# Performance work log

Hardware: AMD Instinct MI355X
Metric: run time of the kernel (lower is better)

Reference implementation:

```python
import jax, jax.numpy as jnp
import numpy as np

NUM_HEADS = 12
N_SAMPLE = 60
COS_LOW = 0.7
COS_HIGH = 0.9
EPS = 1e-12  # F.normalize eps


def _l2norm(x, axis=-1):
    n = jnp.linalg.norm(x, axis=axis, keepdims=True)
    return x / jnp.maximum(n, EPS)


def get_random_attn(rng, v, n_sample, cos_low, cos_high):
    # v: (B, S) -- the CLS attention-score row per batch-head
    norm = jnp.linalg.norm(v, axis=-1, keepdims=True)            # (B, 1)
    u = _l2norm(v)                                               # (B, S)
    u = jnp.broadcast_to(u[None], (n_sample,) + v.shape)         # (n, B, S)
    k1, k2 = jax.random.split(rng)
    r = jax.random.uniform(k1, u.shape, dtype=v.dtype) * 2 - 1   # (n, B, S)
    a = jnp.einsum('nbd,nbd->nb', r, u)[..., None]               # (n, B, 1)
    uperp = _l2norm(r - a * u)                                   # (n, B, S)
    cos = (jax.random.uniform(k2, (n_sample,), dtype=v.dtype)
           * (cos_high - cos_low) + cos_low)[:, None, None]      # (n, 1, 1)
    w = cos * u + jnp.sqrt(1 - cos ** 2) * uperp                 # (n, B, S)
    return jnp.transpose(w * norm[None], (1, 0, 2))              # (B, n, S)


def setup_inputs() -> dict:
    key = jax.random.key(0)
    ks = jax.random.split(key, 8)
    L, N, E = 197, 128, 768
    s = 0.02
    return {
        'query': jax.random.normal(ks[0], (L, N, E), jnp.float32),
        'key': jax.random.normal(ks[1], (L, N, E), jnp.float32),
        'value': jax.random.normal(ks[2], (L, N, E), jnp.float32),
        'in_proj_weight': jax.random.normal(ks[3], (3 * E, E), jnp.float32) * s,
        'in_proj_bias': jax.random.normal(ks[4], (3 * E,), jnp.float32) * s,
        'out_proj_weight': jax.random.normal(ks[5], (E, E), jnp.float32) * s,
        'out_proj_bias': jax.random.normal(ks[6], (E,), jnp.float32) * s,
    }


def reference(query, key, value, in_proj_weight, in_proj_bias,
              out_proj_weight, out_proj_bias):
    L, N, E = query.shape
    H = NUM_HEADS
    hd = E // H
    # packed in-projection (separate q/k/v tensors -> chunked weights)
    w_q, w_k, w_v = jnp.split(in_proj_weight, 3, axis=0)
    b_q, b_k, b_v = jnp.split(in_proj_bias, 3, axis=0)
    q = query @ w_q.T + b_q
    k = key @ w_k.T + b_k
    v = value @ w_v.T + b_v
    # (L, N, E) -> (N*H, L, hd)
    q = jnp.transpose(q.reshape(L, N * H, hd), (1, 0, 2))
    k = jnp.transpose(k.reshape(L, N * H, hd), (1, 0, 2))
    v = jnp.transpose(v.reshape(L, N * H, hd), (1, 0, 2))
    q = q / jnp.sqrt(jnp.asarray(hd, q.dtype))
    attn = jnp.einsum('bte,bse->bts', q, k)                      # (B, L, S)
    center = attn[:, 0, :]                                        # (B, S)
    rand_rows = get_random_attn(jax.random.key(1234), center,
                                N_SAMPLE, COS_LOW, COS_HIGH)      # (B, n, S)
    attn = jnp.concatenate([attn[:, :1, :], rand_rows, attn[:, 1:, :]], axis=1)
    attn = jax.nn.softmax(attn, axis=-1)                          # (B, L+n, S)
    out = jnp.einsum('bts,bse->bte', attn, v)                     # (B, L+n, hd)
    Lt = L + N_SAMPLE
    out = jnp.transpose(out, (1, 0, 2)).reshape(Lt, N, E)
    out = out @ out_proj_weight.T + out_proj_bias                 # (Lt, N, E)
    attn_weights = attn.reshape(N, H, Lt, L).mean(axis=1)         # averaged heads
    return out, attn_weights
```

## Files before the change

### kernel.cpp

```cpp
#include <hip/hip_runtime.h>
#include <stdint.h>

constexpr int Lc  = 197;
constexpr int Nc  = 128;
constexpr int Ec  = 768;
constexpr int HDc = 64;
constexpr int Bc  = Nc * 12;
constexpr int LTc = Lc + 60;
constexpr float EPSc = 1e-12f;

struct U2 { uint32_t x, y; };

__device__ __forceinline__ U2 tf2x32(uint32_t k0, uint32_t k1, uint32_t x0, uint32_t x1) {
  uint32_t k2 = k0 ^ k1 ^ 0x1BD11BDAu;
  x0 += k0; x1 += k1;
#define TFR(r) { x0 += x1; x1 = (x1 << (r)) | (x1 >> (32 - (r))); x1 ^= x0; }
  TFR(13) TFR(15) TFR(26) TFR(6)
  x0 += k1; x1 += k2 + 1u;
  TFR(17) TFR(29) TFR(16) TFR(24)
  x0 += k2; x1 += k0 + 2u;
  TFR(13) TFR(15) TFR(26) TFR(6)
  x0 += k0; x1 += k1 + 3u;
  TFR(17) TFR(29) TFR(16) TFR(24)
  x0 += k1; x1 += k2 + 4u;
  TFR(13) TFR(15) TFR(26) TFR(6)
  x0 += k2; x1 += k0 + 5u;
#undef TFR
  return {x0, x1};
}

__device__ __forceinline__ float u01f(uint32_t bits) {
  return __uint_as_float((bits >> 9) | 0x3f800000u) - 1.0f;
}

__device__ __forceinline__ uint32_t rbits(uint32_t ka, uint32_t kb, uint32_t idx) {
  U2 r = tf2x32(ka, kb, 0u, idx);
  return r.x ^ r.y;
}

__device__ __forceinline__ void split_keys(uint32_t& k1a, uint32_t& k1b, uint32_t& k2a, uint32_t& k2b) {
  U2 t0 = tf2x32(0u, 1234u, 0u, 0u); k1a = t0.x; k1b = t0.y;
  U2 t1 = tf2x32(0u, 1234u, 0u, 1u); k2a = t1.x; k2b = t1.y;
}

__device__ __forceinline__ float rdlane(float v, int l) {
  return __int_as_float(__builtin_amdgcn_readlane(__float_as_int(v), l));
}

__device__ __forceinline__ void f2hilo(float f, unsigned short& h, unsigned short& l) {
  uint32_t u = __float_as_uint(f);
  h = (unsigned short)(u >> 16);
  float lof = f - __uint_as_float(u & 0xffff0000u);
  l = (unsigned short)(__float_as_uint(lof) >> 16);
}

__global__ __launch_bounds__(256) void convert_hilo(const float* __restrict__ src,
                                                    unsigned short* __restrict__ dst,
                                                    int rows)
{
  int idx = blockIdx.x * 256 + threadIdx.x;
  int total = rows * 192;
  if (idx >= total) return;
  int m = idx / 192, c = (idx % 192) * 4;
  float4 f = *(const float4*)(src + (size_t)m * 768 + c);
  ushort4 hv, lv;
  f2hilo(f.x, hv.x, lv.x);
  f2hilo(f.y, hv.y, lv.y);
  f2hilo(f.z, hv.z, lv.z);
  f2hilo(f.w, hv.w, lv.w);
  *(ushort4*)(dst + (size_t)m * 1536 + c) = hv;
  *(ushort4*)(dst + (size_t)m * 1536 + 768 + c) = lv;
}

typedef __attribute__((ext_vector_type(8))) short bfrag_t;
typedef __attribute__((ext_vector_type(4))) float accfrag_t;

template <int MODE>
__global__ __launch_bounds__(256) void gemm_mfma(
    const unsigned short* __restrict__ A0, const unsigned short* __restrict__ A1,
    const unsigned short* __restrict__ A2in, const unsigned short* __restrict__ Wb,
    const float* __restrict__ bias, int cb,
    float* __restrict__ O0, float* __restrict__ O1, float* __restrict__ O2)
{
  __shared__ unsigned short As[128 * 40];
  __shared__ unsigned short Bs[128 * 40];
  const int bm = blockIdx.x;
  const int bn = cb + blockIdx.y;
  const int tid = threadIdx.x;
  const int lane = tid & 63, wv = tid >> 6;
  const int wm = (wv & 1) * 64, wn = (wv >> 1) * 64;
  const int q4 = lane >> 4, l16 = lane & 15;

  const unsigned short* A;
  int which = 0;
  if (MODE == 0) { which = bn / 6; A = which == 0 ? A0 : (which == 1 ? A1 : A2in); }
  else A = A0;

  const int sr = tid >> 2;
  const int sc = (tid & 3) * 8;

  accfrag_t acc[4][4];
#pragma unroll
  for (int i = 0; i < 4; i++)
#pragma unroll
    for (int j = 0; j < 4; j++)
#pragma unroll
      for (int r = 0; r < 4; r++) acc[i][j][r] = 0.0f;

  for (int kt = 0; kt < 48; kt++) {
    const int k0 = kt * 32;
    __syncthreads();
#pragma unroll
    for (int p = 0; p < 2; p++) {
      int r = p * 64 + sr;
      uint4 av = *(const uint4*)(A  + (size_t)(bm * 128 + r) * 1536 + k0 + sc);
      *(uint4*)&As[r * 40 + sc] = av;
      uint4 bv = *(const uint4*)(Wb + (size_t)(bn * 128 + r) * 1536 + k0 + sc);
      *(uint4*)&Bs[r * 40 + sc] = bv;
    }
    __syncthreads();
    bfrag_t af[4], bf[4];
#pragma unroll
    for (int i = 0; i < 4; i++) {
      af[i] = *(const bfrag_t*)&As[(wm + i * 16 + l16) * 40 + q4 * 8];
      bf[i] = *(const bfrag_t*)&Bs[(wn + i * 16 + l16) * 40 + q4 * 8];
    }
#pragma unroll
    for (int i = 0; i < 4; i++)
#pragma unroll
      for (int j = 0; j < 4; j++)
        acc[i][j] = __builtin_amdgcn_mfma_f32_16x16x32_bf16(af[i], bf[j], acc[i][j], 0, 0, 0);
  }

  float bv4[4];
#pragma unroll
  for (int j = 0; j < 4; j++) bv4[j] = bias[bn * 128 + wn + j * 16 + l16];

  if (MODE == 0) {
    const float scale = (which == 0) ? 0.125f : 1.0f;
    float* O = which == 0 ? O0 : (which == 1 ? O1 : O2);
#pragma unroll
    for (int i = 0; i < 4; i++) {
#pragma unroll
      for (int r = 0; r < 4; r++) {
        int m = bm * 128 + wm + i * 16 + q4 * 4 + r;
        int l = m >> 7, nb = m & 127;
#pragma unroll
        for (int j = 0; j < 4; j++) {
          int ng = bn * 128 + wn + j * 16 + l16;
          int nc = ng - which * 768;
          int h = nc >> 6, d = nc & 63;
          O[(((size_t)(nb * 12 + h)) * 197 + l) * 64 + d] = (acc[i][j][r] + bv4[j]) * scale;
        }
      }
    }
  } else {
#pragma unroll
    for (int i = 0; i < 4; i++) {
#pragma unroll
      for (int r = 0; r < 4; r++) {
        int m = bm * 128 + wm + i * 16 + q4 * 4 + r;
#pragma unroll
        for (int j = 0; j < 4; j++) {
          int ng = bn * 128 + wn + j * 16 + l16;
          O0[(size_t)m * 768 + ng] = acc[i][j][r] + bv4[j];
        }
      }
    }
  }
}

__global__ __launch_bounds__(256) void center_kernel(
    const float* __restrict__ q_ws, const float* __restrict__ k_ws,
    float* __restrict__ center, float* __restrict__ cnorm)
{
  const int b = blockIdx.x;
  const int lane = threadIdx.x & 63, w = threadIdx.x >> 6;
  __shared__ float ssh[4];
  const float q0 = q_ws[(size_t)b * (197 * 64) + lane];
  float ss = 0.0f;
  for (int s = w; s < 197; s += 4) {
    float val = q0 * k_ws[((size_t)b * 197 + s) * 64 + lane];
#pragma unroll
    for (int off = 32; off >= 1; off >>= 1) val += __shfl_xor(val, off, 64);
    if (lane == 0) center[(size_t)b * 197 + s] = val;
    ss += val * val;
  }
  if (lane == 0) ssh[w] = ss;
  __syncthreads();
  if (threadIdx.x == 0) cnorm[b] = sqrtf(ssh[0] + ssh[1] + ssh[2] + ssh[3]);
}

__device__ __forceinline__ void softmax_row(float x0, float x1, float x2, float x3,
                                            bool v3, float* p)
{
  float m = fmaxf(fmaxf(x0, x1), x2);
  if (v3) m = fmaxf(m, x3);
#pragma unroll
  for (int off = 32; off >= 1; off >>= 1) m = fmaxf(m, __shfl_xor(m, off, 64));
  float e0 = __expf(x0 - m), e1 = __expf(x1 - m), e2 = __expf(x2 - m);
  float e3 = v3 ? __expf(x3 - m) : 0.0f;
  float s = e0 + e1 + e2 + e3;
#pragma unroll
  for (int off = 32; off >= 1; off >>= 1) s += __shfl_xor(s, off, 64);
  float rs = 1.0f / s;
  p[0] = e0 * rs; p[1] = e1 * rs; p[2] = e2 * rs; p[3] = e3 * rs;
}

__device__ __forceinline__ void softmax4(float x[4][4], bool v3, float p[4][4])
{
  float m[4], s[4];
#pragma unroll
  for (int i = 0; i < 4; i++) {
    m[i] = fmaxf(fmaxf(x[i][0], x[i][1]), x[i][2]);
    if (v3) m[i] = fmaxf(m[i], x[i][3]);
  }
#pragma unroll
  for (int off = 32; off >= 1; off >>= 1) {
#pragma unroll
    for (int i = 0; i < 4; i++) m[i] = fmaxf(m[i], __shfl_xor(m[i], off, 64));
  }
#pragma unroll
  for (int i = 0; i < 4; i++) {
    float e0 = __expf(x[i][0] - m[i]);
    float e1 = __expf(x[i][1] - m[i]);
    float e2 = __expf(x[i][2] - m[i]);
    float e3 = v3 ? __expf(x[i][3] - m[i]) : 0.0f;
    p[i][0] = e0; p[i][1] = e1; p[i][2] = e2; p[i][3] = e3;
    s[i] = e0 + e1 + e2 + e3;
  }
#pragma unroll
  for (int off = 32; off >= 1; off >>= 1) {
#pragma unroll
    for (int i = 0; i < 4; i++) s[i] += __shfl_xor(s[i], off, 64);
  }
#pragma unroll
  for (int i = 0; i < 4; i++) {
    float rs = 1.0f / s[i];
    p[i][0] *= rs; p[i][1] *= rs; p[i][2] *= rs; p[i][3] *= rs;
  }
}

__device__ __forceinline__ void weights_add(float* __restrict__ awn, int t, int lane,
                                            bool v3, const float* p)
{
  float* a = awn + (size_t)t * 197;
  const float c = 1.0f / 12.0f;
  atomicAdd(a + lane, p[0] * c);
  atomicAdd(a + lane + 64, p[1] * c);
  atomicAdd(a + lane + 128, p[2] * c);
  if (v3) atomicAdd(a + lane + 192, p[3] * c);
}

__device__ __forceinline__ void pv_store4(const float* __restrict__ vg, float p[4][4],
                                          int t0, int nval, int n, int h, int lane,
                                          unsigned short* __restrict__ A2)
{
  float o[4] = {0.0f, 0.0f, 0.0f, 0.0f};
#pragma unroll
  for (int j = 0; j < 4; j++) {
    const int send = (j < 3) ? 64 : 5;
#pragma unroll 4
    for (int si = 0; si < send; si++) {
      const int s = j * 64 + si;
      float vv = vg[(size_t)s * 64 + lane];
      o[0] = fmaf(rdlane(p[0][j], si), vv, o[0]);
      o[1] = fmaf(rdlane(p[1][j], si), vv, o[1]);
      o[2] = fmaf(rdlane(p[2][j], si), vv, o[2]);
      o[3] = fmaf(rdlane(p[3][j], si), vv, o[3]);
    }
  }
#pragma unroll
  for (int i = 0; i < 4; i++) {
    if (i < nval) {
      unsigned short hb, lb;
      f2hilo(o[i], hb, lb);
      size_t base = ((size_t)(t0 + i) * 128 + n) * 1536 + h * 64 + lane;
      A2[base] = hb;
      A2[base + 768] = lb;
    }
  }
}

__global__ __launch_bounds__(512, 6) void attn_kernel(
    const float* __restrict__ q_ws, const float* __restrict__ k_ws, const float* __restrict__ v_ws,
    const float* __restrict__ center, const float* __restrict__ cnorm,
    unsigned short* __restrict__ A2, float* __restrict__ attn_w)
{
  __shared__ float kT[64][201];
  __shared__ float cen[200];
  __shared__ float uu[200];

  const int b = blockIdx.x;
  const int n = b / 12, h = b % 12;
  const int tid = threadIdx.x;
  const int lane = tid & 63, w = tid >> 6;
  const bool v3 = lane < 5;

  const float* kg = k_ws + (size_t)b * (197 * 64);
  const float* vg = v_ws + (size_t)b * (197 * 64);
  const float* qg = q_ws + (size_t)b * (197 * 64);

  for (int idx = tid; idx < 197 * 64; idx += 512)
    kT[idx & 63][idx >> 6] = kg[idx];
  {
    float inv = 1.0f / fmaxf(cnorm[b], EPSc);
    for (int s = tid; s < 197; s += 512) {
      float c = center[(size_t)b * 197 + s];
      cen[s] = c;
      uu[s] = c * inv;
    }
  }
  __syncthreads();

  const float us0 = uu[lane], us1 = uu[lane + 64], us2 = uu[lane + 128];
  const float us3 = v3 ? uu[lane + 192] : 0.0f;

  const float cnb = cnorm[b];
  uint32_t k1a, k1b, k2a, k2b;
  split_keys(k1a, k1b, k2a, k2b);
  float* awn = attn_w + (size_t)n * (LTc * 197);

  for (int g = w; g < 16; g += 8) {
    const int t0 = g * 4;
    const int nval = (g == 15) ? 1 : 4;
    float pr[4][4];
#pragma unroll
    for (int i = 0; i < 4; i++) {
      if (i >= nval) { pr[i][0] = pr[i][1] = pr[i][2] = pr[i][3] = 0.0f; continue; }
      const int t = t0 + i;
      float x0, x1, x2, x3;
      if (t == 0) {
        x0 = cen[lane]; x1 = cen[lane + 64]; x2 = cen[lane + 128];
        x3 = v3 ? cen[lane + 192] : 0.0f;
      } else {
        const int ns = t - 1;
        const uint32_t base = ((uint32_t)ns * 1536u + (uint32_t)b) * 197u;
        float r0 = u01f(rbits(k1a, k1b, base + lane))       * 2.0f - 1.0f;
        float r1 = u01f(rbits(k1a, k1b, base + lane + 64))  * 2.0f - 1.0f;
        float r2 = u01f(rbits(k1a, k1b, base + lane + 128)) * 2.0f - 1.0f;
        float r3 = v3 ? (u01f(rbits(k1a, k1b, base + lane + 192)) * 2.0f - 1.0f) : 0.0f;
        float pa = r0 * us0 + r1 * us1 + r2 * us2 + r3 * us3;
#pragma unroll
        for (int off = 32; off >= 1; off >>= 1) pa += __shfl_xor(pa, off, 64);
        float rp0 = r0 - pa * us0, rp1 = r1 - pa * us1;
        float rp2 = r2 - pa * us2, rp3 = r3 - pa * us3;
        float sq2 = rp0 * rp0 + rp1 * rp1 + rp2 * rp2 + (v3 ? rp3 * rp3 : 0.0f);
#pragma unroll
        for (int off = 32; off >= 1; off >>= 1) sq2 += __shfl_xor(sq2, off, 64);
        float invn = 1.0f / fmaxf(sqrtf(sq2), EPSc);
        float cv = u01f(rbits(k2a, k2b, (uint32_t)ns)) * 0.2f + 0.7f;
        float sv = sqrtf(1.0f - cv * cv);
        float f = sv * invn;
        x0 = cnb * (cv * us0 + f * rp0);
        x1 = cnb * (cv * us1 + f * rp1);
        x2 = cnb * (cv * us2 + f * rp2);
        x3 = cnb * (cv * us3 + f * rp3);
      }
      softmax_row(x0, x1, x2, x3, v3, pr[i]);
      weights_add(awn, t, lane, v3, pr[i]);
    }
    pv_store4(vg, pr, t0, nval, n, h, lane, A2);
  }

  for (int bi = w; bi < 49; bi += 8) {
    const int t0 = 61 + bi * 4;
    const int l0 = t0 - 60;
    float qr[4];
#pragma unroll
    for (int i = 0; i < 4; i++)
      qr[i] = qg[(size_t)(l0 + i) * 64 + lane];

    float acc[4][4] = {};
#pragma unroll 4
    for (int d = 0; d < 64; d++) {
      float q0 = rdlane(qr[0], d), q1 = rdlane(qr[1], d);
      float q2 = rdlane(qr[2], d), q3 = rdlane(qr[3], d);
      float kv0 = kT[d][lane], kv1 = kT[d][lane + 64], kv2 = kT[d][lane + 128];
      float kv3 = v3 ? kT[d][lane + 192] : 0.0f;
      acc[0][0] = fmaf(q0, kv0, acc[0][0]); acc[0][1] = fmaf(q0, kv1, acc[0][1]);
      acc[0][2] = fmaf(q0, kv2, acc[0][2]); acc[0][3] = fmaf(q0, kv3, acc[0][3]);
      acc[1][0] = fmaf(q1, kv0, acc[1][0]); acc[1][1] = fmaf(q1, kv1, acc[1][1]);
      acc[1][2] = fmaf(q1, kv2, acc[1][2]); acc[1][3] = fmaf(q1, kv3, acc[1][3]);
      acc[2][0] = fmaf(q2, kv0, acc[2][0]); acc[2][1] = fmaf(q2, kv1, acc[2][1]);
      acc[2][2] = fmaf(q2, kv2, acc[2][2]); acc[2][3] = fmaf(q2, kv3, acc[2][3]);
      acc[3][0] = fmaf(q3, kv0, acc[3][0]); acc[3][1] = fmaf(q3, kv1, acc[3][1]);
      acc[3][2] = fmaf(q3, kv2, acc[3][2]); acc[3][3] = fmaf(q3, kv3, acc[3][3]);
    }
    float pr[4][4];
    softmax4(acc, v3, pr);
#pragma unroll
    for (int i = 0; i < 4; i++)
      weights_add(awn, t0 + i, lane, v3, pr[i]);
    pv_store4(vg, pr, t0, 4, n, h, lane, A2);
  }
}

extern "C" void kernel_launch(void* const* d_in, const int* in_sizes, int n_in,
                              void* d_out, int out_size, void* d_ws, size_t ws_size,
                              hipStream_t stream)
{
  const float* query = (const float*)d_in[0];
  const float* key   = (const float*)d_in[1];
  const float* value = (const float*)d_in[2];
  const float* w_in  = (const float*)d_in[3];
  const float* b_in  = (const float*)d_in[4];
  const float* w_out = (const float*)d_in[5];
  const float* b_out = (const float*)d_in[6];

  float* out    = (float*)d_out;
  float* attn_w = out + (size_t)LTc * Nc * Ec;

  constexpr size_t SZ_HEADF = (size_t)Bc * Lc * HDc * 4;
  constexpr size_t OFF_CEN  = 3 * SZ_HEADF;
  constexpr size_t OFF_CN   = OFF_CEN + (size_t)Bc * Lc * 4;
  constexpr size_t R0       = OFF_CN + 8192;
  constexpr size_t SZ_XB    = (size_t)25216 * 1536 * 2;
  constexpr size_t SZ_A2    = (size_t)LTc * Nc * 1536 * 2;
  constexpr size_t SZ_WB    = (size_t)2304 * 1536 * 2;
  constexpr size_t SZ_WOB   = (size_t)768 * 1536 * 2;
  constexpr size_t FULL_NEED = R0 + 3 * SZ_XB + SZ_WB + SZ_WOB;

  uint8_t* w8 = (uint8_t*)d_ws;
  float* q_ws   = (float*)w8;
  float* k_ws   = (float*)(w8 + SZ_HEADF);
  float* v_ws   = (float*)(w8 + 2 * SZ_HEADF);
  float* center = (float*)(w8 + OFF_CEN);
  float* cnorm  = (float*)(w8 + OFF_CN);
  unsigned short* A2b = (unsigned short*)(w8 + R0);

  const bool full = ws_size >= FULL_NEED;
  unsigned short* wb  = (unsigned short*)(w8 + (full ? (R0 + 3 * SZ_XB) : (R0 + SZ_XB)));
  unsigned short* wob = (unsigned short*)(w8 + (full ? (R0 + 3 * SZ_XB + SZ_WB) : (R0 + SZ_A2)));

  (void)in_sizes; (void)n_in; (void)out_size;

  convert_hilo<<<(2304 * 192 + 255) / 256, 256, 0, stream>>>(w_in, wb, 2304);
  convert_hilo<<<(768 * 192 + 255) / 256, 256, 0, stream>>>(w_out, wob, 768);

  const int xblk = (25216 * 192 + 255) / 256;
  if (full) {
    unsigned short* xb0 = (unsigned short*)(w8 + R0);
    unsigned short* xb1 = xb0 + SZ_XB / 2;
    unsigned short* xb2 = xb1 + SZ_XB / 2;
    convert_hilo<<<xblk, 256, 0, stream>>>(query, xb0, 25216);
    convert_hilo<<<xblk, 256, 0, stream>>>(key,   xb1, 25216);
    convert_hilo<<<xblk, 256, 0, stream>>>(value, xb2, 25216);
    gemm_mfma<0><<<dim3(197, 18), 256, 0, stream>>>(xb0, xb1, xb2, wb, b_in, 0,
                                                    q_ws, k_ws, v_ws);
  } else {
    unsigned short* buf = (unsigned short*)(w8 + R0);
    const float* xs[3] = {query, key, value};
    for (int wh = 0; wh < 3; wh++) {
      convert_hilo<<<xblk, 256, 0, stream>>>(xs[wh], buf, 25216);
      gemm_mfma<0><<<dim3(197, 6), 256, 0, stream>>>(buf, buf, buf, wb, b_in, 6 * wh,
                                                     q_ws, k_ws, v_ws);
    }
  }

  center_kernel<<<dim3(1536), 256, 0, stream>>>(q_ws, k_ws, center, cnorm);

  hipMemsetAsync(attn_w, 0, (size_t)Nc * LTc * Lc * sizeof(float), stream);

  attn_kernel<<<dim3(1536), 512, 0, stream>>>(q_ws, k_ws, v_ws, center, cnorm,
                                              A2b, attn_w);

  gemm_mfma<1><<<dim3(257, 6), 256, 0, stream>>>(A2b, nullptr, nullptr, wob, b_out, 0,
                                                 out, nullptr, nullptr);
}
```

Baseline: 1.571 ms.

## Compute P·V with bf16 MFMA using split-hi/lo V tiles in LDS

```diff
diff --git a/kernel.cpp b/kernel.cpp
--- a/kernel.cpp
+++ b/kernel.cpp
@@ -54,6 +54,12 @@
   l = (unsigned short)(__float_as_uint(lof) >> 16);
 }
 
+__device__ __forceinline__ unsigned short bf16rne(float f) {
+  uint32_t u = __float_as_uint(f);
+  u += 0x7fffu + ((u >> 16) & 1u);
+  return (unsigned short)(u >> 16);
+}
+
 __global__ __launch_bounds__(256) void convert_hilo(const float* __restrict__ src,
                                                     unsigned short* __restrict__ dst,
                                                     int rows)
@@ -191,22 +197,6 @@
   if (threadIdx.x == 0) cnorm[b] = sqrtf(ssh[0] + ssh[1] + ssh[2] + ssh[3]);
 }
 
-__device__ __forceinline__ void softmax_row(float x0, float x1, float x2, float x3,
-                                            bool v3, float* p)
-{
-  float m = fmaxf(fmaxf(x0, x1), x2);
-  if (v3) m = fmaxf(m, x3);
-#pragma unroll
-  for (int off = 32; off >= 1; off >>= 1) m = fmaxf(m, __shfl_xor(m, off, 64));
-  float e0 = __expf(x0 - m), e1 = __expf(x1 - m), e2 = __expf(x2 - m);
-  float e3 = v3 ? __expf(x3 - m) : 0.0f;
-  float s = e0 + e1 + e2 + e3;
-#pragma unroll
-  for (int off = 32; off >= 1; off >>= 1) s += __shfl_xor(s, off, 64);
-  float rs = 1.0f / s;
-  p[0] = e0 * rs; p[1] = e1 * rs; p[2] = e2 * rs; p[3] = e3 * rs;
-}
-
 __device__ __forceinline__ void softmax4(float x[4][4], bool v3, float p[4][4])
 {
   float m[4], s[4];
@@ -252,42 +242,15 @@
   if (v3) atomicAdd(a + lane + 192, p[3] * c);
 }
 
-__device__ __forceinline__ void pv_store4(const float* __restrict__ vg, float p[4][4],
-                                          int t0, int nval, int n, int h, int lane,
-                                          unsigned short* __restrict__ A2)
-{
-  float o[4] = {0.0f, 0.0f, 0.0f, 0.0f};
-#pragma unroll
-  for (int j = 0; j < 4; j++) {
-    const int send = (j < 3) ? 64 : 5;
-#pragma unroll 4
-    for (int si = 0; si < send; si++) {
-      const int s = j * 64 + si;
-      float vv = vg[(size_t)s * 64 + lane];
-      o[0] = fmaf(rdlane(p[0][j], si), vv, o[0]);
-      o[1] = fmaf(rdlane(p[1][j], si), vv, o[1]);
-      o[2] = fmaf(rdlane(p[2][j], si), vv, o[2]);
-      o[3] = fmaf(rdlane(p[3][j], si), vv, o[3]);
-    }
-  }
-#pragma unroll
-  for (int i = 0; i < 4; i++) {
-    if (i < nval) {
-      unsigned short hb, lb;
-      f2hilo(o[i], hb, lb);
-      size_t base = ((size_t)(t0 + i) * 128 + n) * 1536 + h * 64 + lane;
-      A2[base] = hb;
-      A2[base + 768] = lb;
-    }
-  }
-}
-
-__global__ __launch_bounds__(512, 6) void attn_kernel(
+__global__ __launch_bounds__(512, 2) void attn_kernel(
     const float* __restrict__ q_ws, const float* __restrict__ k_ws, const float* __restrict__ v_ws,
     const float* __restrict__ center, const float* __restrict__ cnorm,
     unsigned short* __restrict__ A2, float* __restrict__ attn_w)
 {
   __shared__ float kT[64][201];
+  __shared__ __align__(16) unsigned short Vth[64 * 232];
+  __shared__ __align__(16) unsigned short Vtl[64 * 232];
+  __shared__ __align__(16) unsigned short Pl[32 * 232];
   __shared__ float cen[200];
   __shared__ float uu[200];
 
@@ -295,14 +258,31 @@
   const int n = b / 12, h = b % 12;
   const int tid = threadIdx.x;
   const int lane = tid & 63, w = tid >> 6;
+  const int q4 = lane >> 4, l16 = lane & 15;
   const bool v3 = lane < 5;
 
   const float* kg = k_ws + (size_t)b * (197 * 64);
   const float* vg = v_ws + (size_t)b * (197 * 64);
   const float* qg = q_ws + (size_t)b * (197 * 64);
 
-  for (int idx = tid; idx < 197 * 64; idx += 512)
-    kT[idx & 63][idx >> 6] = kg[idx];
+  for (int idx = tid; idx < 64 * 35; idx += 512) {
+    int d = idx / 35, s = 197 + idx % 35;
+    Vth[d * 232 + s] = 0;
+    Vtl[d * 232 + s] = 0;
+  }
+  for (int idx = tid; idx < 32 * 35; idx += 512) {
+    int r = idx / 35, s = 197 + idx % 35;
+    Pl[r * 232 + s] = 0;
+  }
+
+  for (int idx = tid; idx < 197 * 64; idx += 512) {
+    int s = idx >> 6, d = idx & 63;
+    kT[d][s] = kg[idx];
+    unsigned short vh, vl;
+    f2hilo(vg[idx], vh, vl);
+    Vth[d * 232 + s] = vh;
+    Vtl[d * 232 + s] = vl;
+  }
   {
     float inv = 1.0f / fmaxf(cnorm[b], EPSc);
     for (int s = tid; s < 197; s += 512) {
@@ -321,78 +301,119 @@
   split_keys(k1a, k1b, k2a, k2b);
   float* awn = attn_w + (size_t)n * (LTc * 197);
 
-  for (int g = w; g < 16; g += 8) {
-    const int t0 = g * 4;
-    const int nval = (g == 15) ? 1 : 4;
-    float pr[4][4];
-#pragma unroll
-    for (int i = 0; i < 4; i++) {
-      if (i >= nval) { pr[i][0] = pr[i][1] = pr[i][2] = pr[i][3] = 0.0f; continue; }
-      const int t = t0 + i;
-      float x0, x1, x2, x3;
-      if (t == 0) {
-        x0 = cen[lane]; x1 = cen[lane + 64]; x2 = cen[lane + 128];
-        x3 = v3 ? cen[lane + 192] : 0.0f;
-      } else {
-        const int ns = t - 1;
-        const uint32_t base = ((uint32_t)ns * 1536u + (uint32_t)b) * 197u;
-        float r0 = u01f(rbits(k1a, k1b, base + lane))       * 2.0f - 1.0f;
-        float r1 = u01f(rbits(k1a, k1b, base + lane + 64))  * 2.0f - 1.0f;
-        float r2 = u01f(rbits(k1a, k1b, base + lane + 128)) * 2.0f - 1.0f;
-        float r3 = v3 ? (u01f(rbits(k1a, k1b, base + lane + 192)) * 2.0f - 1.0f) : 0.0f;
-        float pa = r0 * us0 + r1 * us1 + r2 * us2 + r3 * us3;
-#pragma unroll
-        for (int off = 32; off >= 1; off >>= 1) pa += __shfl_xor(pa, off, 64);
-        float rp0 = r0 - pa * us0, rp1 = r1 - pa * us1;
-        float rp2 = r2 - pa * us2, rp3 = r3 - pa * us3;
-        float sq2 = rp0 * rp0 + rp1 * rp1 + rp2 * rp2 + (v3 ? rp3 * rp3 : 0.0f);
-#pragma unroll
-        for (int off = 32; off >= 1; off >>= 1) sq2 += __shfl_xor(sq2, off, 64);
-        float invn = 1.0f / fmaxf(sqrtf(sq2), EPSc);
-        float cv = u01f(rbits(k2a, k2b, (uint32_t)ns)) * 0.2f + 0.7f;
-        float sv = sqrtf(1.0f - cv * cv);
-        float f = sv * invn;
-        x0 = cnb * (cv * us0 + f * rp0);
-        x1 = cnb * (cv * us1 + f * rp1);
-        x2 = cnb * (cv * us2 + f * rp2);
-        x3 = cnb * (cv * us3 + f * rp3);
-      }
-      softmax_row(x0, x1, x2, x3, v3, pr[i]);
-      weights_add(awn, t, lane, v3, pr[i]);
-    }
-    pv_store4(vg, pr, t0, nval, n, h, lane, A2);
-  }
-
-  for (int bi = w; bi < 49; bi += 8) {
-    const int t0 = 61 + bi * 4;
-    const int l0 = t0 - 60;
-    float qr[4];
-#pragma unroll
-    for (int i = 0; i < 4; i++)
-      qr[i] = qg[(size_t)(l0 + i) * 64 + lane];
-
-    float acc[4][4] = {};
+  for (int c = 0; c < 9; c++) {
+    const int t0 = c * 32 + w * 4;
+    const bool sact = (c < 8) || (w == 0);
+
+    if (sact) {
+      float x[4][4];
+      if (t0 + 3 >= 61) {
+        float qr[4];
+#pragma unroll
+        for (int i = 0; i < 4; i++) {
+          int l = t0 + i - 60;
+          l = l < 0 ? 0 : (l > 196 ? 196 : l);
+          qr[i] = qg[(size_t)l * 64 + lane];
+        }
+#pragma unroll
+        for (int i = 0; i < 4; i++)
+#pragma unroll
+          for (int j = 0; j < 4; j++) x[i][j] = 0.0f;
 #pragma unroll 4
-    for (int d = 0; d < 64; d++) {
-      float q0 = rdlane(qr[0], d), q1 = rdlane(qr[1], d);
-      float q2 = rdlane(qr[2], d), q3 = rdlane(qr[3], d);
-      float kv0 = kT[d][lane], kv1 = kT[d][lane + 64], kv2 = kT[d][lane + 128];
-      float kv3 = v3 ? kT[d][lane + 192] : 0.0f;
-      acc[0][0] = fmaf(q0, kv0, acc[0][0]); acc[0][1] = fmaf(q0, kv1, acc[0][1]);
-      acc[0][2] = fmaf(q0, kv2, acc[0][2]); acc[0][3] = fmaf(q0, kv3, acc[0][3]);
-      acc[1][0] = fmaf(q1, kv0, acc[1][0]); acc[1][1] = fmaf(q1, kv1, acc[1][1]);
-      acc[1][2] = fmaf(q1, kv2, acc[1][2]); acc[1][3] = fmaf(q1, kv3, acc[1][3]);
-      acc[2][0] = fmaf(q2, kv0, acc[2][0]); acc[2][1] = fmaf(q2, kv1, acc[2][1]);
-      acc[2][2] = fmaf(q2, kv2, acc[2][2]); acc[2][3] = fmaf(q2, kv3, acc[2][3]);
-      acc[3][0] = fmaf(q3, kv0, acc[3][0]); acc[3][1] = fmaf(q3, kv1, acc[3][1]);
-      acc[3][2] = fmaf(q3, kv2, acc[3][2]); acc[3][3] = fmaf(q3, kv3, acc[3][3]);
-    }
-    float pr[4][4];
-    softmax4(acc, v3, pr);
-#pragma unroll
-    for (int i = 0; i < 4; i++)
-      weights_add(awn, t0 + i, lane, v3, pr[i]);
-    pv_store4(vg, pr, t0, 4, n, h, lane, A2);
+        for (int d = 0; d < 64; d++) {
+          float q0 = rdlane(qr[0], d), q1 = rdlane(qr[1], d);
+          float q2 = rdlane(qr[2], d), q3 = rdlane(qr[3], d);
+          float kv0 = kT[d][lane], kv1 = kT[d][lane + 64], kv2 = kT[d][lane + 128];
+          float kv3 = v3 ? kT[d][lane + 192] : 0.0f;
+          x[0][0] = fmaf(q0, kv0, x[0][0]); x[0][1] = fmaf(q0, kv1, x[0][1]);
+          x[0][2] = fmaf(q0, kv2, x[0][2]); x[0][3] = fmaf(q0, kv3, x[0][3]);
+          x[1][0] = fmaf(q1, kv0, x[1][0]); x[1][1] = fmaf(q1, kv1, x[1][1]);
+          x[1][2] = fmaf(q1, kv2, x[1][2]); x[1][3] = fmaf(q1, kv3, x[1][3]);
+          x[2][0] = fmaf(q2, kv0, x[2][0]); x[2][1] = fmaf(q2, kv1, x[2][1]);
+          x[2][2] = fmaf(q2, kv2, x[2][2]); x[2][3] = fmaf(q2, kv3, x[2][3]);
+          x[3][0] = fmaf(q3, kv0, x[3][0]); x[3][1] = fmaf(q3, kv1, x[3][1]);
+          x[3][2] = fmaf(q3, kv2, x[3][2]); x[3][3] = fmaf(q3, kv3, x[3][3]);
+        }
+      }
+#pragma unroll
+      for (int i = 0; i < 4; i++) {
+        const int t = t0 + i;
+        if (t >= 61) continue;
+        if (t == 0) {
+          x[0][0] = cen[lane]; x[0][1] = cen[lane + 64]; x[0][2] = cen[lane + 128];
+          x[0][3] = v3 ? cen[lane + 192] : 0.0f;
+        } else {
+          const int ns = t - 1;
+          const uint32_t base = ((uint32_t)ns * 1536u + (uint32_t)b) * 197u;
+          float r0 = u01f(rbits(k1a, k1b, base + lane))       * 2.0f - 1.0f;
+          float r1 = u01f(rbits(k1a, k1b, base + lane + 64))  * 2.0f - 1.0f;
+          float r2 = u01f(rbits(k1a, k1b, base + lane + 128)) * 2.0f - 1.0f;
+          float r3 = v3 ? (u01f(rbits(k1a, k1b, base + lane + 192)) * 2.0f - 1.0f) : 0.0f;
+          float pa = r0 * us0 + r1 * us1 + r2 * us2 + r3 * us3;
+#pragma unroll
+          for (int off = 32; off >= 1; off >>= 1) pa += __shfl_xor(pa, off, 64);
+          float rp0 = r0 - pa * us0, rp1 = r1 - pa * us1;
+          float rp2 = r2 - pa * us2, rp3 = r3 - pa * us3;
+          float sq2 = rp0 * rp0 + rp1 * rp1 + rp2 * rp2 + (v3 ? rp3 * rp3 : 0.0f);
+#pragma unroll
+          for (int off = 32; off >= 1; off >>= 1) sq2 += __shfl_xor(sq2, off, 64);
+          float invn = 1.0f / fmaxf(sqrtf(sq2), EPSc);
+          float cv = u01f(rbits(k2a, k2b, (uint32_t)ns)) * 0.2f + 0.7f;
+          float sv = sqrtf(1.0f - cv * cv);
+          float f = sv * invn;
+          x[i][0] = cnb * (cv * us0 + f * rp0);
+          x[i][1] = cnb * (cv * us1 + f * rp1);
+          x[i][2] = cnb * (cv * us2 + f * rp2);
+          x[i][3] = cnb * (cv * us3 + f * rp3);
+        }
+      }
+      float pr[4][4];
+      softmax4(x, v3, pr);
+#pragma unroll
+      for (int i = 0; i < 4; i++)
+        if (c < 8 || i == 0) weights_add(awn, t0 + i, lane, v3, pr[i]);
+#pragma unroll
+      for (int i = 0; i < 4; i++) {
+        unsigned short* pRow = Pl + (w * 4 + i) * 232;
+        pRow[lane]       = bf16rne(pr[i][0]);
+        pRow[lane + 64]  = bf16rne(pr[i][1]);
+        pRow[lane + 128] = bf16rne(pr[i][2]);
+        if (v3) pRow[lane + 192] = bf16rne(pr[i][3]);
+      }
+    }
+    __syncthreads();
+
+    const bool pvact = (c < 8) || (w < 4);
+    if (pvact) {
+      const int tt = (c < 8) ? (w >> 2) : 0;
+      const int dj = (c < 8) ? (w & 3) : w;
+      accfrag_t acc = {0.0f, 0.0f, 0.0f, 0.0f};
+      const unsigned short* pA = Pl  + (tt * 16 + l16) * 232 + q4 * 8;
+      const unsigned short* pH = Vth + (dj * 16 + l16) * 232 + q4 * 8;
+      const unsigned short* pL = Vtl + (dj * 16 + l16) * 232 + q4 * 8;
+#pragma unroll
+      for (int ks = 0; ks < 7; ks++) {
+        bfrag_t af = *(const bfrag_t*)(pA + ks * 32);
+        bfrag_t bh = *(const bfrag_t*)(pH + ks * 32);
+        bfrag_t bl = *(const bfrag_t*)(pL + ks * 32);
+        acc = __builtin_amdgcn_mfma_f32_16x16x32_bf16(af, bh, acc, 0, 0, 0);
+        acc = __builtin_amdgcn_mfma_f32_16x16x32_bf16(af, bl, acc, 0, 0, 0);
+      }
+      const int tbase = c * 32 + tt * 16 + q4 * 4;
+      const int d = dj * 16 + l16;
+#pragma unroll
+      for (int r = 0; r < 4; r++) {
+        const int t = tbase + r;
+        if (t <= 256) {
+          unsigned short hb, lb;
+          f2hilo(acc[r], hb, lb);
+          size_t base = ((size_t)t * 128 + n) * 1536 + h * 64 + d;
+          A2[base] = hb;
+          A2[base + 768] = lb;
+        }
+      }
+    }
+    __syncthreads();
   }
 }
 
```

Result: faster. 1.428 ms (-9.1%).
